# Optimization experiments

Hardware: AMD Instinct MI355X
Metric: run time of the kernel (lower is better)

## Reference

```python
import jax, jax.numpy as jnp
import numpy as np

RC = 4.6  # cutoff radius (Angstrom), from init_kwargs
FACTOR = 7.199822675975224  # constants.half_Hartree * constants.Bohr (eV*A)


def exp_cutoff(d, rc):
    # smooth exponential (bump) cutoff: exp(1 - 1/(1-(d/rc)^2)) for d<rc, else 0
    x = d / rc
    inside = x < 1.0
    xs = jnp.where(inside, x, 0.5)  # safe value to avoid nan in masked branch
    f = jnp.exp(1.0 - 1.0 / (1.0 - xs * xs))
    return jnp.where(inside, f, 0.0)


def setup_inputs() -> dict:
    key = jax.random.key(0)
    k1, k2 = jax.random.split(key)
    B, N = 64, 512
    # atoms in a 40 A box -> realistic long-range distances
    coord = jax.random.uniform(k1, (B, N, 3), dtype=jnp.float32) * 40.0
    charges = jax.random.normal(k2, (B, N), dtype=jnp.float32) * 0.3
    mask = jnp.ones((B, N), dtype=bool)  # all atoms valid (no padding)
    return {"coord": coord, "charges": charges, "mask": mask}


def reference(coord, charges, mask):
    # coul_simple: e = factor * sum_ij (1 - fc(d_ij)) * q_i * q_j / d_ij, per molecule
    B, N, _ = coord.shape
    pair_mask = mask[:, :, None] & mask[:, None, :]
    eye = jnp.eye(N, dtype=bool)[None]
    valid = pair_mask & ~eye  # mask self-pairs and padding (mask_ij_)
    disp = coord[:, :, None, :] - coord[:, None, :, :]          # [B,N,N,3]
    d2 = jnp.sum(disp * disp, axis=-1)                          # [B,N,N]
    d = jnp.sqrt(jnp.where(valid, d2, 1.0))                     # safe sqrt on diag
    fc = 1.0 - exp_cutoff(d, RC)
    qq = charges[:, :, None] * charges[:, None, :]              # q_i * q_j
    e_ij = jnp.where(valid, fc * qq / d, 0.0)
    return FACTOR * jnp.sum(e_ij, axis=(1, 2))                  # mol_sum -> [B]
```

## Files before the change

### kernel.cpp

```cpp
#include <hip/hip_runtime.h>

#define N_ATOMS 512
#define NTILE   8
#define BLOCK   256
#define FACTOR  7.199822675975224f
#define RC2f    (4.6f * 4.6f)

__global__ __launch_bounds__(BLOCK) void coul_pair_kernel(
    const float* __restrict__ coord,
    const float* __restrict__ charges,
    float* __restrict__ partials)
{
    const int b = blockIdx.x >> 3;
    const int c = blockIdx.x & 7;

    __shared__ float4 atom[N_ATOMS];

    const float* co = coord   + (size_t)b * N_ATOMS * 3;
    const float* q  = charges + (size_t)b * N_ATOMS;
    for (int k = threadIdx.x; k < N_ATOMS; k += BLOCK)
        atom[k] = make_float4(co[3 * k], co[3 * k + 1], co[3 * k + 2], q[k]);
    __syncthreads();

    const int t    = threadIdx.x;
    const int w    = t >> 6;
    const int lane = t & 63;
    const float4 ai = atom[(c << 6) + lane];

    float accM = 0.0f;
    float accS = 0.0f;

    {
        const float4* __restrict__ base = &atom[((c + w + 1) & 7) << 6];
        #pragma unroll 8
        for (int k = 0; k < 64; ++k) {
            const float4 aj = base[k];
            float dx = ai.x - aj.x, dy = ai.y - aj.y, dz = ai.z - aj.z;
            float d2 = dx * dx + dy * dy + dz * dz;
            float r  = __builtin_amdgcn_rsqf(d2);
            float tv = aj.w * r;
            accM += tv;
            if (d2 < RC2f) {
                float uu = __builtin_amdgcn_rcpf(RC2f - d2);
                float e  = __expf(-d2 * uu);
                accM -= tv * e;
            }
        }
    }
    {
        const int kk0 = w << 4;
        const float4* __restrict__ base = &atom[(c << 6) + kk0];
        #pragma unroll
        for (int k = 0; k < 16; ++k) {
            const float4 aj = base[k];
            float dx = ai.x - aj.x, dy = ai.y - aj.y, dz = ai.z - aj.z;
            float d2 = dx * dx + dy * dy + dz * dz;
            float r  = __builtin_amdgcn_rsqf(d2);
            float tv = (kk0 + k == lane) ? 0.0f : aj.w * r;
            accS += tv;
            if (d2 < RC2f) {
                float uu = __builtin_amdgcn_rcpf(RC2f - d2);
                float e  = __expf(-d2 * uu);
                accS -= tv * e;
            }
        }
    }

    float acc = ((w == 3) ? 0.5f * accM : accM) + 0.5f * accS;
    acc *= ai.w;

    #pragma unroll
    for (int off = 32; off > 0; off >>= 1)
        acc += __shfl_down(acc, off, 64);

    __shared__ float wsum[BLOCK / 64];
    if ((t & 63) == 0) wsum[t >> 6] = acc;
    __syncthreads();
    if (t == 0)
        partials[blockIdx.x] = wsum[0] + wsum[1] + wsum[2] + wsum[3];
}

__global__ void coul_reduce_kernel(const float* __restrict__ partials,
                                   float* __restrict__ out, int B)
{
    const int b = threadIdx.x;
    if (b < B) {
        float sum = 0.0f;
        #pragma unroll
        for (int s = 0; s < NTILE; ++s) sum += partials[b * NTILE + s];
        out[b] = 2.0f * FACTOR * sum;
    }
}

extern "C" void kernel_launch(void* const* d_in, const int* in_sizes, int n_in,
                              void* d_out, int out_size, void* d_ws, size_t ws_size,
                              hipStream_t stream) {
    const float* coord   = (const float*)d_in[0];
    const float* charges = (const float*)d_in[1];
    float* out      = (float*)d_out;
    float* partials = (float*)d_ws;

    const int B = (n_in > 2 && in_sizes[1] != in_sizes[2])
                      ? in_sizes[1] / (N_ATOMS * 4)
                      : in_sizes[1] / N_ATOMS;

    coul_pair_kernel<<<B * NTILE, BLOCK, 0, stream>>>(coord, charges, partials);
    coul_reduce_kernel<<<1, 64, 0, stream>>>(partials, out, B);
}
```

Measured before the change: 65.49 us.

## Use one 1024-thread block per molecule and drop the separate reduce kernel

Changes the work split from eight 256-thread blocks per molecule to one 1024-thread block per molecule. Each of the 16 wavefronts handles a 64-atom tile against two off-diagonal tiles and half of its diagonal tile. The final reduction moves into the block, so the second kernel launch and the global partials buffer go away. The cost is a shared-memory atom load done once per block instead of eight times, but only 64 blocks, which may underfill the 256 CUs of the GPU.

```diff
diff --git a/kernel.cpp b/kernel.cpp
--- a/kernel.cpp
+++ b/kernel.cpp
@@ -1,72 +1,85 @@
 #include <hip/hip_runtime.h>
 
 #define N_ATOMS 512
-#define NTILE   8
-#define BLOCK   256
+#define BLOCK   1024
 #define FACTOR  7.199822675975224f
 #define RC2f    (4.6f * 4.6f)
 
-__global__ __launch_bounds__(BLOCK) void coul_pair_kernel(
+__global__ __launch_bounds__(BLOCK) void coul_mol_kernel(
     const float* __restrict__ coord,
     const float* __restrict__ charges,
-    float* __restrict__ partials)
+    float* __restrict__ out)
 {
-    const int b = blockIdx.x >> 3;
-    const int c = blockIdx.x & 7;
+    const int b = blockIdx.x;
+    const int t = threadIdx.x;
 
     __shared__ float4 atom[N_ATOMS];
 
     const float* co = coord   + (size_t)b * N_ATOMS * 3;
     const float* q  = charges + (size_t)b * N_ATOMS;
-    for (int k = threadIdx.x; k < N_ATOMS; k += BLOCK)
-        atom[k] = make_float4(co[3 * k], co[3 * k + 1], co[3 * k + 2], q[k]);
+    if (t < N_ATOMS)
+        atom[t] = make_float4(co[3 * t], co[3 * t + 1], co[3 * t + 2], q[t]);
     __syncthreads();
 
-    const int t    = threadIdx.x;
     const int w    = t >> 6;
     const int lane = t & 63;
+    const int c    = w & 7;
+    const int h    = w >> 3;
     const float4 ai = atom[(c << 6) + lane];
 
-    float accM = 0.0f;
+    float accA = 0.0f;
+    float accB = 0.0f;
     float accS = 0.0f;
 
     {
-        const float4* __restrict__ base = &atom[((c + w + 1) & 7) << 6];
+        const float4* __restrict__ base = &atom[((c + 1 + 2 * h) & 7) << 6];
         #pragma unroll 8
         for (int k = 0; k < 64; ++k) {
             const float4 aj = base[k];
             float dx = ai.x - aj.x, dy = ai.y - aj.y, dz = ai.z - aj.z;
             float d2 = dx * dx + dy * dy + dz * dz;
-            float r  = __builtin_amdgcn_rsqf(d2);
-            float tv = aj.w * r;
-            accM += tv;
+            float tv = aj.w * __builtin_amdgcn_rsqf(d2);
+            accA += tv;
             if (d2 < RC2f) {
                 float uu = __builtin_amdgcn_rcpf(RC2f - d2);
-                float e  = __expf(-d2 * uu);
-                accM -= tv * e;
+                accA -= tv * __expf(-d2 * uu);
             }
         }
     }
     {
-        const int kk0 = w << 4;
-        const float4* __restrict__ base = &atom[(c << 6) + kk0];
-        #pragma unroll
-        for (int k = 0; k < 16; ++k) {
+        const float4* __restrict__ base = &atom[((c + 2 + 2 * h) & 7) << 6];
+        #pragma unroll 8
+        for (int k = 0; k < 64; ++k) {
+            const float4 aj = base[k];
+            float dx = ai.x - aj.x, dy = ai.y - aj.y, dz = ai.z - aj.z;
+            float d2 = dx * dx + dy * dy + dz * dz;
+            float tv = aj.w * __builtin_amdgcn_rsqf(d2);
+            accB += tv;
+            if (d2 < RC2f) {
+                float uu = __builtin_amdgcn_rcpf(RC2f - d2);
+                accB -= tv * __expf(-d2 * uu);
+            }
+        }
+    }
+    {
+        const int k0 = h << 5;
+        const float4* __restrict__ base = &atom[(c << 6) + k0];
+        #pragma unroll 8
+        for (int k = 0; k < 32; ++k) {
             const float4 aj = base[k];
             float dx = ai.x - aj.x, dy = ai.y - aj.y, dz = ai.z - aj.z;
             float d2 = dx * dx + dy * dy + dz * dz;
             float r  = __builtin_amdgcn_rsqf(d2);
-            float tv = (kk0 + k == lane) ? 0.0f : aj.w * r;
+            float tv = (k0 + k == lane) ? 0.0f : aj.w * r;
             accS += tv;
             if (d2 < RC2f) {
                 float uu = __builtin_amdgcn_rcpf(RC2f - d2);
-                float e  = __expf(-d2 * uu);
-                accS -= tv * e;
+                accS -= tv * __expf(-d2 * uu);
             }
         }
     }
 
-    float acc = ((w == 3) ? 0.5f * accM : accM) + 0.5f * accS;
+    float acc = accA + (h ? 0.5f : 1.0f) * accB + 0.5f * accS;
     acc *= ai.w;
 
     #pragma unroll
@@ -76,18 +89,10 @@
     __shared__ float wsum[BLOCK / 64];
     if ((t & 63) == 0) wsum[t >> 6] = acc;
     __syncthreads();
-    if (t == 0)
-        partials[blockIdx.x] = wsum[0] + wsum[1] + wsum[2] + wsum[3];
-}
-
-__global__ void coul_reduce_kernel(const float* __restrict__ partials,
-                                   float* __restrict__ out, int B)
-{
-    const int b = threadIdx.x;
-    if (b < B) {
+    if (t == 0) {
         float sum = 0.0f;
         #pragma unroll
-        for (int s = 0; s < NTILE; ++s) sum += partials[b * NTILE + s];
+        for (int v = 0; v < BLOCK / 64; ++v) sum += wsum[v];
         out[b] = 2.0f * FACTOR * sum;
     }
 }
@@ -97,13 +102,12 @@
                               hipStream_t stream) {
     const float* coord   = (const float*)d_in[0];
     const float* charges = (const float*)d_in[1];
-    float* out      = (float*)d_out;
-    float* partials = (float*)d_ws;
+    float* out = (float*)d_out;
+    (void)d_ws; (void)ws_size;
 
     const int B = (n_in > 2 && in_sizes[1] != in_sizes[2])
                       ? in_sizes[1] / (N_ATOMS * 4)
                       : in_sizes[1] / N_ATOMS;
 
-    coul_pair_kernel<<<B * NTILE, BLOCK, 0, stream>>>(coord, charges, partials);
-    coul_reduce_kernel<<<1, 64, 0, stream>>>(partials, out, B);
+    coul_mol_kernel<<<B, BLOCK, 0, stream>>>(coord, charges, out);
 }
```

After: 78.26 us. 1.2x slower.

## Split pair work into 16 blocks per molecule with finer j-chunk distribution

Applied to the files above, without the earlier changes.

Doubles the grid from 8 to 16 blocks per molecule. Each block now covers half of the j-range for its i-tile: every wave handles an 8-atom slice of each of three full off-diagonal tiles, the half-weighted opposite tile, and the diagonal tile. The reduce kernel reads 16 partials per molecule with float4 loads. The goal is more parallelism across the GPU's compute units, at the cost of each block loading the full molecule into shared memory twice as often and doing less work per block.

```diff
diff --git a/kernel.cpp b/kernel.cpp
--- a/kernel.cpp
+++ b/kernel.cpp
@@ -1,7 +1,7 @@
 #include <hip/hip_runtime.h>
 
 #define N_ATOMS 512
-#define NTILE   8
+#define SPLITS  16
 #define BLOCK   256
 #define FACTOR  7.199822675975224f
 #define RC2f    (4.6f * 4.6f)
@@ -11,63 +11,81 @@
     const float* __restrict__ charges,
     float* __restrict__ partials)
 {
-    const int b = blockIdx.x >> 3;
+    const int b = blockIdx.x >> 4;
     const int c = blockIdx.x & 7;
+    const int p = (blockIdx.x >> 3) & 1;
 
     __shared__ float4 atom[N_ATOMS];
 
     const float* co = coord   + (size_t)b * N_ATOMS * 3;
     const float* q  = charges + (size_t)b * N_ATOMS;
-    for (int k = threadIdx.x; k < N_ATOMS; k += BLOCK)
+    const int t = threadIdx.x;
+    {
+        int k = t;
         atom[k] = make_float4(co[3 * k], co[3 * k + 1], co[3 * k + 2], q[k]);
+        k += BLOCK;
+        atom[k] = make_float4(co[3 * k], co[3 * k + 1], co[3 * k + 2], q[k]);
+    }
     __syncthreads();
 
-    const int t    = threadIdx.x;
     const int w    = t >> 6;
     const int lane = t & 63;
+    const int u8   = (p * 4 + w) * 8;
     const float4 ai = atom[(c << 6) + lane];
 
-    float accM = 0.0f;
+    float accF = 0.0f;
+    float accH = 0.0f;
     float accS = 0.0f;
 
+    #pragma unroll
+    for (int seg = 0; seg < 3; ++seg) {
+        const float4* __restrict__ base = &atom[(((c + 1 + seg) & 7) << 6) + u8];
+        #pragma unroll
+        for (int k = 0; k < 8; ++k) {
+            const float4 aj = base[k];
+            float dx = ai.x - aj.x, dy = ai.y - aj.y, dz = ai.z - aj.z;
+            float d2 = dx * dx + dy * dy + dz * dz;
+            float tv = aj.w * __builtin_amdgcn_rsqf(d2);
+            accF += tv;
+            if (d2 < RC2f) {
+                float uu = __builtin_amdgcn_rcpf(RC2f - d2);
+                accF -= tv * __expf(-d2 * uu);
+            }
+        }
+    }
     {
-        const float4* __restrict__ base = &atom[((c + w + 1) & 7) << 6];
-        #pragma unroll 8
-        for (int k = 0; k < 64; ++k) {
+        const float4* __restrict__ base = &atom[(((c + 4) & 7) << 6) + u8];
+        #pragma unroll
+        for (int k = 0; k < 8; ++k) {
+            const float4 aj = base[k];
+            float dx = ai.x - aj.x, dy = ai.y - aj.y, dz = ai.z - aj.z;
+            float d2 = dx * dx + dy * dy + dz * dz;
+            float tv = aj.w * __builtin_amdgcn_rsqf(d2);
+            accH += tv;
+            if (d2 < RC2f) {
+                float uu = __builtin_amdgcn_rcpf(RC2f - d2);
+                accH -= tv * __expf(-d2 * uu);
+            }
+        }
+    }
+    {
+        const float4* __restrict__ base = &atom[(c << 6) + u8];
+        #pragma unroll
+        for (int k = 0; k < 8; ++k) {
             const float4 aj = base[k];
             float dx = ai.x - aj.x, dy = ai.y - aj.y, dz = ai.z - aj.z;
             float d2 = dx * dx + dy * dy + dz * dz;
             float r  = __builtin_amdgcn_rsqf(d2);
-            float tv = aj.w * r;
-            accM += tv;
-            if (d2 < RC2f) {
-                float uu = __builtin_amdgcn_rcpf(RC2f - d2);
-                float e  = __expf(-d2 * uu);
-                accM -= tv * e;
-            }
-        }
-    }
-    {
-        const int kk0 = w << 4;
-        const float4* __restrict__ base = &atom[(c << 6) + kk0];
-        #pragma unroll
-        for (int k = 0; k < 16; ++k) {
-            const float4 aj = base[k];
-            float dx = ai.x - aj.x, dy = ai.y - aj.y, dz = ai.z - aj.z;
-            float d2 = dx * dx + dy * dy + dz * dz;
-            float r  = __builtin_amdgcn_rsqf(d2);
-            float tv = (kk0 + k == lane) ? 0.0f : aj.w * r;
+            float tv = (u8 + k == lane) ? 0.0f : aj.w * r;
             accS += tv;
             if (d2 < RC2f) {
                 float uu = __builtin_amdgcn_rcpf(RC2f - d2);
-                float e  = __expf(-d2 * uu);
-                accS -= tv * e;
+                accS -= tv * __expf(-d2 * uu);
             }
         }
     }
 
-    float acc = ((w == 3) ? 0.5f * accM : accM) + 0.5f * accS;
-    acc *= ai.w;
+    float acc = (accF + 0.5f * (accH + accS)) * ai.w;
 
     #pragma unroll
     for (int off = 32; off > 0; off >>= 1)
@@ -85,9 +103,13 @@
 {
     const int b = threadIdx.x;
     if (b < B) {
-        float sum = 0.0f;
-        #pragma unroll
-        for (int s = 0; s < NTILE; ++s) sum += partials[b * NTILE + s];
+        const float4* p4 =
+            reinterpret_cast<const float4*>(partials) + b * (SPLITS / 4);
+        float4 v0 = p4[0], v1 = p4[1], v2 = p4[2], v3 = p4[3];
+        float sum = (v0.x + v0.y + v0.z + v0.w)
+                  + (v1.x + v1.y + v1.z + v1.w)
+                  + (v2.x + v2.y + v2.z + v2.w)
+                  + (v3.x + v3.y + v3.z + v3.w);
         out[b] = 2.0f * FACTOR * sum;
     }
 }
@@ -104,6 +126,6 @@
                       ? in_sizes[1] / (N_ATOMS * 4)
                       : in_sizes[1] / N_ATOMS;
 
-    coul_pair_kernel<<<B * NTILE, BLOCK, 0, stream>>>(coord, charges, partials);
+    coul_pair_kernel<<<B * SPLITS, BLOCK, 0, stream>>>(coord, charges, partials);
     coul_reduce_kernel<<<1, 64, 0, stream>>>(partials, out, B);
 }
```

New measurement: 64.81 us. About the same (-1.0%).
